# Kernel tuning notes

Hardware: AMD Instinct MI355X
Metric: run time of the kernel (lower is better)

The kernel has to match this reference:

```python
import jax, jax.numpy as jnp
import numpy as np
from jax import lax

B, T, I, H, L = 512, 2048, 16, 40, 3

def setup_inputs() -> dict:
    key = jax.random.key(0)
    ks = jax.random.split(key, 4 * L + 3)
    bound = 1.0 / np.sqrt(H)
    u = lambda k, shp: jax.random.uniform(k, shp, jnp.float32, -bound, bound)
    inp = {"x": jax.random.normal(ks[0], (B, T, I), jnp.float32)}
    for l in range(L):
        in_dim = I if l == 0 else H
        inp[f"w_ih{l}"] = u(ks[1 + 4 * l], (H, in_dim))
        inp[f"w_hh{l}"] = u(ks[2 + 4 * l], (H, H))
        inp[f"b_ih{l}"] = u(ks[3 + 4 * l], (H,))
        inp[f"b_hh{l}"] = u(ks[4 + 4 * l], (H,))
    inp["fc_w"] = u(ks[4 * L + 1], (1, H))
    inp["fc_b"] = u(ks[4 * L + 2], (1,))
    return inp

def _rnn_layer(x_seq, w_ih, w_hh, b_ih, b_hh):
    # Precompute input projection as one big GEMM: [B, T, H]
    xp = jnp.einsum('bti,hi->bth', x_seq, w_ih) + b_ih + b_hh
    h0 = jnp.zeros((x_seq.shape[0], w_hh.shape[0]), x_seq.dtype)
    def step(h, xt):  # xt: [B, H]
        h = jnp.tanh(xt + h @ w_hh.T)
        return h, h
    _, ys = lax.scan(step, h0, jnp.swapaxes(xp, 0, 1))  # [T, B, H]
    return jnp.swapaxes(ys, 0, 1)  # [B, T, H]

def reference(x, w_ih0, w_hh0, b_ih0, b_hh0,
              w_ih1, w_hh1, b_ih1, b_hh1,
              w_ih2, w_hh2, b_ih2, b_hh2, fc_w, fc_b):
    # Multi-layer tanh RNN (eval mode: inter-layer and final dropout are identity)
    h = _rnn_layer(x, w_ih0, w_hh0, b_ih0, b_hh0)
    h = _rnn_layer(h, w_ih1, w_hh1, b_ih1, b_hh1)
    h = _rnn_layer(h, w_ih2, w_hh2, b_ih2, b_hh2)
    last = h[:, -1, :]                     # [B, H]
    out = last @ fc_w.T + fc_b             # [B, 1]
    return out[:, 0]                       # [B]
```

## Files before the change

### kernel.cpp

```cpp
#include <hip/hip_runtime.h>
#include <cstddef>
#include <cstdint>

#define B_ 512
#define T_ 2048
#define I_ 16
#define H_ 40

typedef __fp16 half_t;
typedef half_t h2 __attribute__((ext_vector_type(2)));
typedef half_t h8 __attribute__((ext_vector_type(8)));
typedef float f4 __attribute__((ext_vector_type(4)));

__device__ __forceinline__ float fast_tanh(float x) {
  float e = __builtin_amdgcn_exp2f(x * 2.8853900817779268f);
  return 1.0f - 2.0f * __builtin_amdgcn_rcpf(e + 1.0f);
}

__device__ __forceinline__ float dot2(h2 a, h2 b, float c) {
#if __has_builtin(__builtin_amdgcn_fdot2)
  return __builtin_amdgcn_fdot2(a, b, c, false);
#else
  return c + (float)a[0] * (float)b[0] + (float)a[1] * (float)b[1];
#endif
}

__device__ __forceinline__ h2 cvtpk(float lo, float hi) {
  h2 r;
  asm volatile("v_cvt_pkrtz_f16_f32 %0, %1, %2" : "=v"(r) : "v"(lo), "v"(hi));
  return r;
}

#define PIN(v) asm volatile("" : "+v"(v))

#define GLOAD16(R0, R1, R2, R3, P)                                  \
  asm volatile("global_load_dwordx4 %0, %4, off\n\t"                \
               "global_load_dwordx4 %1, %4, off offset:16\n\t"      \
               "global_load_dwordx4 %2, %4, off offset:32\n\t"      \
               "global_load_dwordx4 %3, %4, off offset:48"          \
               : "=&v"(R0), "=&v"(R1), "=&v"(R2), "=&v"(R3)         \
               : "v"(P))

#define WAITX(N)                                                    \
  do {                                                              \
    asm volatile("s_waitcnt vmcnt(" #N ")" ::: "memory");           \
    __builtin_amdgcn_sched_barrier(0);                              \
  } while (0)

#define LOADW(DST, SRC, STR, N2)                                    \
  _Pragma("unroll") for (int k = 0; k < (N2); ++k) {                \
    DST[k][0] = (half_t)SRC[jr * (STR) + 2 * k];                    \
    DST[k][1] = (half_t)SRC[jr * (STR) + 2 * k + 1];                \
    PIN(DST[k]);                                                    \
  }

#define HD(HP, W)                                                   \
  do {                                                              \
    _Pragma("unroll") for (int m = 0; m < 5; ++m) {                 \
      h8 q = (HP)[m];                                               \
      h2 p0 = {q[0], q[1]}, p1 = {q[2], q[3]};                      \
      h2 p2 = {q[4], q[5]}, p3 = {q[6], q[7]};                      \
      a0 = dot2(p0, (W)[4 * m + 0], a0);                            \
      a1 = dot2(p1, (W)[4 * m + 1], a1);                            \
      a2 = dot2(p2, (W)[4 * m + 2], a2);                            \
      a3 = dot2(p3, (W)[4 * m + 3], a3);                            \
    }                                                               \
  } while (0)

#define STEP(XH)                                                    \
  do {                                                              \
    const h8* hp0 = (const h8*)&hb16[0][0];                         \
    const h8* hp1 = (const h8*)&hb16[1][0];                         \
    const h8* hp2 = (const h8*)&hb16[2][0];                         \
                                             \
    float a0 = bias0, a1 = 0.f, a2 = 0.f, a3 = 0.f;                 \
    a0 = dot2(XH[0], w0i[0], a0); a1 = dot2(XH[1], w0i[1], a1);     \
    a2 = dot2(XH[2], w0i[2], a2); a3 = dot2(XH[3], w0i[3], a3);     \
    a0 = dot2(XH[4], w0i[4], a0); a1 = dot2(XH[5], w0i[5], a1);     \
    a2 = dot2(XH[6], w0i[6], a2); a3 = dot2(XH[7], w0i[7], a3);     \
    HD(hp0, w0h);                                       \
    const float nh0 = fast_tanh((a0 + a1) + (a2 + a3));             \
    hb16[0][j] = (half_t)nh0;                                       \
                                             \
    a0 = bias1; a1 = a2 = a3 = 0.f;                                 \
    HD(hp0, w1i);                                       \
    HD(hp1, w1h);                                       \
    const float nh1 = fast_tanh((a0 + a1) + (a2 + a3));             \
    hb16[1][j] = (half_t)nh1;                                       \
                                             \
    a0 = bias2; a1 = a2 = a3 = 0.f;                                 \
    HD(hp1, w2i);                                       \
    HD(hp2, w2h);                                       \
    nh2v = fast_tanh((a0 + a1) + (a2 + a3));                        \
    hb16[2][j] = (half_t)nh2v;                                      \
  } while (0)

#define PACKX(XH, R0, R1, R2, R3)                                   \
  do {                                                              \
    XH[0] = cvtpk(R0[0], R0[1]); XH[1] = cvtpk(R0[2], R0[3]);       \
    XH[2] = cvtpk(R1[0], R1[1]); XH[3] = cvtpk(R1[2], R1[3]);       \
    XH[4] = cvtpk(R2[0], R2[1]); XH[5] = cvtpk(R2[2], R2[3]);       \
    XH[6] = cvtpk(R3[0], R3[1]); XH[7] = cvtpk(R3[2], R3[3]);       \
  } while (0)

__global__ __launch_bounds__(64)
__attribute__((amdgpu_waves_per_eu(1, 1)))
void rnn3_fused(const float* __restrict__ x,
                const float* __restrict__ wih0, const float* __restrict__ whh0,
                const float* __restrict__ bih0, const float* __restrict__ bhh0,
                const float* __restrict__ wih1, const float* __restrict__ whh1,
                const float* __restrict__ b_ih1, const float* __restrict__ bhh1,
                const float* __restrict__ wih2, const float* __restrict__ whh2,
                const float* __restrict__ bih2, const float* __restrict__ bhh2,
                const float* __restrict__ fcw, const float* __restrict__ fcb,
                float* __restrict__ out) {
  const int b = blockIdx.x;
  const int j = threadIdx.x;
  const int jr = (j < H_) ? j : (H_ - 1);

  h2 w0i[I_ / 2], w0h[H_ / 2], w1i[H_ / 2], w1h[H_ / 2], w2i[H_ / 2], w2h[H_ / 2];
  LOADW(w0i, wih0, I_, I_ / 2)
  LOADW(w0h, whh0, H_, H_ / 2)
  LOADW(w1i, wih1, H_, H_ / 2)
  LOADW(w1h, whh1, H_, H_ / 2)
  LOADW(w2i, wih2, H_, H_ / 2)
  LOADW(w2h, whh2, H_, H_ / 2)

  float bias0 = bih0[jr] + bhh0[jr];  PIN(bias0);
  float bias1 = b_ih1[jr] + bhh1[jr]; PIN(bias1);
  float bias2 = bih2[jr] + bhh2[jr];  PIN(bias2);

  __shared__ __align__(16) half_t hb16[3][64];
  hb16[0][j] = (half_t)0.f; hb16[1][j] = (half_t)0.f; hb16[2][j] = (half_t)0.f;
  __syncthreads();

  const float* __restrict__ xb = x + (size_t)b * (T_ * I_);

  f4 rA0, rA1, rA2, rA3, rB0, rB1, rB2, rB3;
  GLOAD16(rA0, rA1, rA2, rA3, xb + 0 * I_);
  GLOAD16(rB0, rB1, rB2, rB3, xb + 1 * I_);

  float nh2v = 0.f;
  h2 xh[8];

  for (int t = 0; t < T_; t += 2) {
    WAITX(4);
    PACKX(xh, rA0, rA1, rA2, rA3);
    STEP(xh);
    { const float* pf = xb + (size_t)((t + 2 < T_) ? t + 2 : T_ - 1) * I_;
      GLOAD16(rA0, rA1, rA2, rA3, pf); }
    WAITX(4);
    PACKX(xh, rB0, rB1, rB2, rB3);
    STEP(xh);
    { const float* pf = xb + (size_t)((t + 3 < T_) ? t + 3 : T_ - 1) * I_;
      GLOAD16(rB0, rB1, rB2, rB3, pf); }
  }

  asm volatile("s_waitcnt vmcnt(0)" ::: "memory");
  __builtin_amdgcn_sched_barrier(0);
  PIN(rA0); PIN(rA1); PIN(rA2); PIN(rA3);
  PIN(rB0); PIN(rB1); PIN(rB2); PIN(rB3);

  const float fw = (j < H_) ? fcw[j] : 0.f;
  float v = nh2v * fw;
#pragma unroll
  for (int off = 32; off > 0; off >>= 1) v += __shfl_down(v, off);
  if (j == 0) out[b] = v + fcb[0];
}

extern "C" void kernel_launch(void* const* d_in, const int* in_sizes, int n_in,
                              void* d_out, int out_size, void* d_ws, size_t ws_size,
                              hipStream_t stream) {
  (void)in_sizes; (void)n_in; (void)d_ws; (void)ws_size; (void)out_size;
  const float* x    = (const float*)d_in[0];
  const float* wih0 = (const float*)d_in[1];
  const float* whh0 = (const float*)d_in[2];
  const float* bih0 = (const float*)d_in[3];
  const float* bhh0 = (const float*)d_in[4];
  const float* wih1 = (const float*)d_in[5];
  const float* whh1 = (const float*)d_in[6];
  const float* bih1 = (const float*)d_in[7];
  const float* bhh1 = (const float*)d_in[8];
  const float* wih2 = (const float*)d_in[9];
  const float* whh2 = (const float*)d_in[10];
  const float* bih2 = (const float*)d_in[11];
  const float* bhh2 = (const float*)d_in[12];
  const float* fcw  = (const float*)d_in[13];
  const float* fcb  = (const float*)d_in[14];
  float* out = (float*)d_out;

  hipLaunchKernelGGL(rnn3_fused, dim3(B_), dim3(64), 0, stream,
                     x, wih0, whh0, bih0, bhh0,
                     wih1, whh1, bih1, bhh1,
                     wih2, whh2, bih2, bhh2,
                     fcw, fcb, out);
}
```

Baseline: 1.106 ms.

## Broadcast hidden state via DPP and readlane instead of LDS

Replaces the shared-memory hidden-state buffer with a cross-lane broadcast. A DPP swap packs adjacent lanes' tanh outputs into fp16 pairs, and readlane copies each pair into 20 scalar-uniform values per layer. This removes LDS writes, reads and their wait latency from the serial recurrence. In exchange it adds 60 readlane operations per step, each converting a vector value to a scalar, which can cost more than the LDS traffic it replaces.

```diff
diff --git a/kernel.cpp b/kernel.cpp
--- a/kernel.cpp
+++ b/kernel.cpp
@@ -9,7 +9,6 @@
 
 typedef __fp16 half_t;
 typedef half_t h2 __attribute__((ext_vector_type(2)));
-typedef half_t h8 __attribute__((ext_vector_type(8)));
 typedef float f4 __attribute__((ext_vector_type(4)));
 
 __device__ __forceinline__ float fast_tanh(float x) {
@@ -18,14 +17,10 @@
 }
 
 __device__ __forceinline__ float dot2(h2 a, h2 b, float c) {
-#if __has_builtin(__builtin_amdgcn_fdot2)
   return __builtin_amdgcn_fdot2(a, b, c, false);
-#else
-  return c + (float)a[0] * (float)b[0] + (float)a[1] * (float)b[1];
-#endif
 }
 
-__device__ __forceinline__ h2 cvtpk(float lo, float hi) {
+__device__ __forceinline__ h2 cvtpk_v(float lo, float hi) {
   h2 r;
   asm volatile("v_cvt_pkrtz_f16_f32 %0, %1, %2" : "=v"(r) : "v"(lo), "v"(hi));
   return r;
@@ -54,53 +49,55 @@
     PIN(DST[k]);                                                    \
   }
 
-#define HD(HP, W)                                                   \
-  do {                                                              \
-    _Pragma("unroll") for (int m = 0; m < 5; ++m) {                 \
-      h8 q = (HP)[m];                                               \
-      h2 p0 = {q[0], q[1]}, p1 = {q[2], q[3]};                      \
-      h2 p2 = {q[4], q[5]}, p3 = {q[6], q[7]};                      \
-      a0 = dot2(p0, (W)[4 * m + 0], a0);                            \
-      a1 = dot2(p1, (W)[4 * m + 1], a1);                            \
-      a2 = dot2(p2, (W)[4 * m + 2], a2);                            \
-      a3 = dot2(p3, (W)[4 * m + 3], a3);                            \
-    }                                                               \
-  } while (0)
+#define BCAST(NH, PAIRS) do {                                       \
+  int nb_ = __builtin_amdgcn_update_dpp(                            \
+      0, __builtin_bit_cast(int, (NH)), 0xB1, 0xf, 0xf, false);     \
+  h2 pk_ = __builtin_amdgcn_cvt_pkrtz((NH),                         \
+      __builtin_bit_cast(float, nb_));                              \
+  int pkb_ = __builtin_bit_cast(int, pk_);                          \
+  _Pragma("unroll") for (int p = 0; p < H_ / 2; ++p)                \
+    PAIRS[p] = __builtin_bit_cast(h2,                               \
+        __builtin_amdgcn_readlane(pkb_, 2 * p));                    \
+} while (0)
 
-#define STEP(XH)                                                    \
-  do {                                                              \
-    const h8* hp0 = (const h8*)&hb16[0][0];                         \
-    const h8* hp1 = (const h8*)&hb16[1][0];                         \
-    const h8* hp2 = (const h8*)&hb16[2][0];                         \
+#define HDS(PAIRS, W, A0, A1, A2, A3)                               \
+  _Pragma("unroll") for (int p = 0; p < 5; ++p) {                   \
+    A0 = dot2(PAIRS[4 * p + 0], (W)[4 * p + 0], A0);                \
+    A1 = dot2(PAIRS[4 * p + 1], (W)[4 * p + 1], A1);                \
+    A2 = dot2(PAIRS[4 * p + 2], (W)[4 * p + 2], A2);                \
+    A3 = dot2(PAIRS[4 * p + 3], (W)[4 * p + 3], A3);                \
+  }
+
+#define STEP(XH) do {                                               \
                                              \
-    float a0 = bias0, a1 = 0.f, a2 = 0.f, a3 = 0.f;                 \
-    a0 = dot2(XH[0], w0i[0], a0); a1 = dot2(XH[1], w0i[1], a1);     \
-    a2 = dot2(XH[2], w0i[2], a2); a3 = dot2(XH[3], w0i[3], a3);     \
-    a0 = dot2(XH[4], w0i[4], a0); a1 = dot2(XH[5], w0i[5], a1);     \
-    a2 = dot2(XH[6], w0i[6], a2); a3 = dot2(XH[7], w0i[7], a3);     \
-    HD(hp0, w0h);                                       \
-    const float nh0 = fast_tanh((a0 + a1) + (a2 + a3));             \
-    hb16[0][j] = (half_t)nh0;                                       \
+  float a0 = bias0, a1 = 0.f, a2 = 0.f, a3 = 0.f;                   \
+  a0 = dot2(XH[0], w0i[0], a0); a1 = dot2(XH[1], w0i[1], a1);       \
+  a2 = dot2(XH[2], w0i[2], a2); a3 = dot2(XH[3], w0i[3], a3);       \
+  a0 = dot2(XH[4], w0i[4], a0); a1 = dot2(XH[5], w0i[5], a1);       \
+  a2 = dot2(XH[6], w0i[6], a2); a3 = dot2(XH[7], w0i[7], a3);       \
+  HDS(hp0, w0h, a0, a1, a2, a3);                        \
+  const float nh0 = fast_tanh((a0 + a1) + (a2 + a3));               \
+  BCAST(nh0, hp0);                                                  \
                                              \
-    a0 = bias1; a1 = a2 = a3 = 0.f;                                 \
-    HD(hp0, w1i);                                       \
-    HD(hp1, w1h);                                       \
-    const float nh1 = fast_tanh((a0 + a1) + (a2 + a3));             \
-    hb16[1][j] = (half_t)nh1;                                       \
+  float b0 = bias1, b1 = 0.f, b2 = 0.f, b3 = 0.f;                   \
+  HDS(hp0, w1i, b0, b1, b2, b3);                        \
+  HDS(hp1, w1h, b0, b1, b2, b3);                        \
+  const float nh1 = fast_tanh((b0 + b1) + (b2 + b3));               \
+  BCAST(nh1, hp1);                                                  \
                                              \
-    a0 = bias2; a1 = a2 = a3 = 0.f;                                 \
-    HD(hp1, w2i);                                       \
-    HD(hp2, w2h);                                       \
-    nh2v = fast_tanh((a0 + a1) + (a2 + a3));                        \
-    hb16[2][j] = (half_t)nh2v;                                      \
-  } while (0)
+  float c0 = bias2, c1 = 0.f, c2 = 0.f, c3 = 0.f;                   \
+  HDS(hp1, w2i, c0, c1, c2, c3);                        \
+  HDS(hp2, w2h, c0, c1, c2, c3);                        \
+  nh2v = fast_tanh((c0 + c1) + (c2 + c3));                          \
+  BCAST(nh2v, hp2);                                                 \
+} while (0)
 
 #define PACKX(XH, R0, R1, R2, R3)                                   \
   do {                                                              \
-    XH[0] = cvtpk(R0[0], R0[1]); XH[1] = cvtpk(R0[2], R0[3]);       \
-    XH[2] = cvtpk(R1[0], R1[1]); XH[3] = cvtpk(R1[2], R1[3]);       \
-    XH[4] = cvtpk(R2[0], R2[1]); XH[5] = cvtpk(R2[2], R2[3]);       \
-    XH[6] = cvtpk(R3[0], R3[1]); XH[7] = cvtpk(R3[2], R3[3]);       \
+    XH[0] = cvtpk_v(R0[0], R0[1]); XH[1] = cvtpk_v(R0[2], R0[3]);   \
+    XH[2] = cvtpk_v(R1[0], R1[1]); XH[3] = cvtpk_v(R1[2], R1[3]);   \
+    XH[4] = cvtpk_v(R2[0], R2[1]); XH[5] = cvtpk_v(R2[2], R2[3]);   \
+    XH[6] = cvtpk_v(R3[0], R3[1]); XH[7] = cvtpk_v(R3[2], R3[3]);   \
   } while (0)
 
 __global__ __launch_bounds__(64)
@@ -130,9 +127,13 @@
   float bias1 = b_ih1[jr] + bhh1[jr]; PIN(bias1);
   float bias2 = bih2[jr] + bhh2[jr];  PIN(bias2);
 
-  __shared__ __align__(16) half_t hb16[3][64];
-  hb16[0][j] = (half_t)0.f; hb16[1][j] = (half_t)0.f; hb16[2][j] = (half_t)0.f;
-  __syncthreads();
+  h2 hp0[H_ / 2], hp1[H_ / 2], hp2[H_ / 2];
+#pragma unroll
+  for (int p = 0; p < H_ / 2; ++p) {
+    hp0[p] = h2{(half_t)0.f, (half_t)0.f};
+    hp1[p] = h2{(half_t)0.f, (half_t)0.f};
+    hp2[p] = h2{(half_t)0.f, (half_t)0.f};
+  }
 
   const float* __restrict__ xb = x + (size_t)b * (T_ * I_);
 
```

After: 926.3 us. -16.3%, faster.
